# Kernel optimization log

Measured on AMD Instinct MI355X. Metric: run time of the kernel, lower is better.

Reference implementation:

```python
import jax, jax.numpy as jnp
import numpy as np

EPS = 1e-7          # keras K.epsilon()
MIN_TEMP = 0.1
ALPHA = 0.99999
START_TEMP = 10.0
BATCH, D, BINS, K_OUT = 4096, 20000, 10, 64


def setup_inputs() -> dict:
    key = jax.random.key(0)
    k1, k2, k3 = jax.random.split(key, 3)
    X = jax.random.normal(k1, (BATCH, D), dtype=jnp.float32)
    u = jax.random.normal(k2, (D, BINS), dtype=jnp.float32)
    # keras 'uniform' initializer: U(-0.05, 0.05)
    tinyW = jax.random.uniform(k3, (BINS, K_OUT), dtype=jnp.float32, minval=-0.05, maxval=0.05)
    temp = jnp.float32(START_TEMP)
    return {"X": X, "u": u, "tinyW": tinyW, "temp": temp}


def greedy_assign(p):
    """Greedy bipartite argmax-and-mask assignment (the host loop in the original).
    p: (k, d) scores. Returns (k, d) 0/1 assignment with one 1 per row, unique cols."""
    k, d = p.shape

    def step(pm, _):
        ind = jnp.argmax(pm)            # global argmax over flattened (k, d)
        x = ind // d
        y = ind % d
        pm = pm.at[x, :].set(-1.0).at[:, y].set(-1.0)
        return pm, (x, y)

    _, (xs, ys) = jax.lax.scan(step, p, None, length=k)
    return jnp.zeros((k, d), p.dtype).at[xs, ys].set(1.0)


def reference(X, u, tinyW, temp):
    # al = softmax(u @ tinyW) over output_dim axis, then transpose -> (k, d)
    al = jax.nn.softmax(u @ tinyW, axis=-1).T                  # (k, d)
    logits = jnp.log(10.0 * jnp.clip(al, EPS, 0.9999999))      # (k, d)
    # Gumbel noise: -log(-log(U)), U ~ Uniform(eps, 1)
    nkey = jax.random.key(42)
    uniform = jax.random.uniform(nkey, logits.shape, logits.dtype, EPS, 1.0)
    gumbel = -jnp.log(-jnp.log(uniform))
    # annealed temperature update (K.update in original)
    new_temp = jnp.maximum(jnp.float32(MIN_TEMP), temp * jnp.float32(ALPHA))
    samples = jax.nn.softmax((logits + gumbel) / new_temp, axis=-1)  # (k, d)
    # inference-path discrete selection via greedy argmax-and-mask loop
    discrete = greedy_assign(samples)                           # (k, d)
    # training path: Y = X @ samples^T  (main memory-bound skinny GEMM)
    Y = X @ samples.T                                           # (batch, k)
    return Y, discrete, new_temp
```

## Files before the change

kernel.cpp:

```cpp
#include <hip/hip_runtime.h>
#include <stdint.h>
#include <math.h>

typedef unsigned long long ull;
typedef __attribute__((ext_vector_type(8))) short short8;
typedef __attribute__((ext_vector_type(4))) float f32x4;

#define DD 20000
#define NK 64
#define NB 4096
#define YN (NB * NK)
#define TOTN (YN + NK * DD + 1)
#define KS 16

#define E_OFF   0u
#define RSP_OFF 10240000u
#define CV_OFF  10400256u
#define CC_OFF  10416640u
#define EB_OFF  10433024u
#define IRS_OFF 12993024u
#define P_OFF   12993280u

__device__ __forceinline__ uint32_t tf_bits(uint32_t j) {
  const uint32_t k0 = 0u, k1 = 42u;
  const uint32_t k2 = 0x1BD11BDAu ^ k0 ^ k1;
  uint32_t x0 = k0;
  uint32_t x1 = j + k1;
#define TFR(r) { x0 += x1; x1 = (x1 << r) | (x1 >> (32 - r)); x1 ^= x0; }
  TFR(13) TFR(15) TFR(26) TFR(6)
  x0 += k1; x1 += k2 + 1u;
  TFR(17) TFR(29) TFR(16) TFR(24)
  x0 += k2; x1 += k0 + 2u;
  TFR(13) TFR(15) TFR(26) TFR(6)
  x0 += k0; x1 += k1 + 3u;
  TFR(17) TFR(29) TFR(16) TFR(24)
  x0 += k1; x1 += k2 + 4u;
  TFR(13) TFR(15) TFR(26) TFR(6)
  x0 += k2; x1 += k0 + 5u;
#undef TFR
  return x0 ^ x1;
}

__global__ __launch_bounds__(256) void k_z(
    const float* __restrict__ uu, const float* __restrict__ tw,
    const float* __restrict__ temp, double* __restrict__ E,
    ushort* __restrict__ EB, double* __restrict__ RSP,
    float* __restrict__ disc) {
  __shared__ double tile[NK][65];
  __shared__ double psumw[4][NK];
  const int tid = threadIdx.x;
  const int lane = tid & 63;
  const int wv = tid >> 6;
  const int d0 = blockIdx.x * 64;
  const float nt = fmaxf(0.1f, temp[0] * 0.99999f);
  float w[10];
#pragma unroll
  for (int i = 0; i < 10; ++i) w[i] = tw[i * NK + lane];
  double psum = 0.0;
  for (int it = 0; it < 16; ++it) {
    const int dl = wv * 16 + it;
    const int d = d0 + dl;
    double e = 0.0;
    if (d < DD) {
      float m = 0.f;
#pragma unroll
      for (int i = 0; i < 10; ++i) m = fmaf(uu[d * 10 + i], w[i], m);
      float mx = m;
#pragma unroll
      for (int off = 32; off; off >>= 1) mx = fmaxf(mx, __shfl_xor(mx, off, 64));
      double ee = exp((double)(m - mx));
      double ssum = ee;
#pragma unroll
      for (int off = 32; off; off >>= 1) ssum += __shfl_xor(ssum, off, 64);
      float al = (float)(ee / ssum);
      float c = fminf(fmaxf(al, 1e-7f), 0.9999999f);
      float lg = (float)log((double)(10.0f * c));
      const uint32_t bits = tf_bits((uint32_t)(lane * DD + d));
      float uf = __uint_as_float((bits >> 9) | 0x3f800000u) - 1.0f;
      float uv = fmaxf(1e-7f, uf * (1.0f - 1e-7f) + 1e-7f);
      float g = (float)(-log(-log((double)uv)));
      float z = (lg + g) / nt;
      e = exp((double)z);
    }
    tile[lane][dl] = e;
    psum += e;
  }
  psumw[wv][lane] = psum;
  __syncthreads();
  for (int r0 = 0; r0 < NK; r0 += 4) {
    const int r = r0 + wv;
    const int d = d0 + lane;
    if (d < DD) {
      const double ev = tile[r][lane];
      E[(size_t)r * DD + d] = ev;
      const float ef = (float)ev;
      uint32_t ub = __float_as_uint(ef);
      EB[(size_t)r * DD + d] = (ushort)((ub + 0x7FFFu + ((ub >> 16) & 1u)) >> 16);
    }
  }
  if (wv == 0) {
    double s = psumw[0][lane] + psumw[1][lane] + psumw[2][lane] + psumw[3][lane];
    RSP[(size_t)blockIdx.x * NK + lane] = s;
  }
  const int cg = tid & 15;
  const int r0 = tid >> 4;
  if (d0 + cg * 4 < DD) {
    for (int r = r0; r < NK; r += 16)
      *(float4*)(disc + (size_t)r * DD + d0 + cg * 4) = make_float4(0.f, 0.f, 0.f, 0.f);
  }
}

__global__ __launch_bounds__(256) void k_rows(
    const double* __restrict__ E, const double* __restrict__ RSP,
    float* __restrict__ cv, int* __restrict__ cc, float* __restrict__ invRS) {
  const int k = blockIdx.x;
  const int tid = threadIdx.x;
  __shared__ double redd[256];
  __shared__ ull keys[2048];
  __shared__ ull wbest[4];
  const double* er = E + (size_t)k * DD;
  double psum = 0.0;
  for (int b = tid; b < 313; b += 256) psum += RSP[(size_t)b * NK + k];
  redd[tid] = psum;
  __syncthreads();
  for (int s = 128; s; s >>= 1) {
    if (tid < s) redd[tid] += redd[tid + s];
    __syncthreads();
  }
  const double sumall = redd[0];
  if (tid == 0) invRS[k] = (float)(1.0 / sumall);
  float tv[8]; int tc[8];
#pragma unroll
  for (int s = 0; s < 8; ++s) { tv[s] = -1.f; tc[s] = 0; }
  for (int d = tid; d < DD; d += 256) {
    float svv = (float)(er[d] / sumall);
    if (svv > tv[7]) {
      float cvr = svv; int ccr = d;
#pragma unroll
      for (int s = 0; s < 8; ++s) {
        bool sw = cvr > tv[s];
        float nv = sw ? cvr : tv[s]; int nc = sw ? ccr : tc[s];
        cvr = sw ? tv[s] : cvr; ccr = sw ? tc[s] : ccr;
        tv[s] = nv; tc[s] = nc;
      }
    }
  }
#pragma unroll
  for (int s = 0; s < 8; ++s)
    keys[(tid << 3) + s] = (((ull)__float_as_uint(tv[s])) << 32)
                         | ((ull)(uint32_t)(32767 - tc[s]) << 11)
                         | ((ull)tid << 3) | (ull)s;
  __syncthreads();
  for (int t = 0; t < NK; ++t) {
    ull best = 0;
#pragma unroll
    for (int s = 0; s < 8; ++s) { ull kk = keys[(tid << 3) + s]; if (kk > best) best = kk; }
#pragma unroll
    for (int off = 32; off; off >>= 1) { ull o = __shfl_xor(best, off, 64); if (o > best) best = o; }
    if ((tid & 63) == 0) wbest[tid >> 6] = best;
    __syncthreads();
    ull win = wbest[0];
#pragma unroll
    for (int wI = 1; wI < 4; ++wI) if (wbest[wI] > win) win = wbest[wI];
    const uint32_t lo = (uint32_t)win;
    const int slot = lo & 7;
    const int owner = (lo >> 3) & 255;
    const int col = 32767 - (int)(lo >> 11);
    if (tid == 0) {
      cv[(k << 6) + t] = __uint_as_float((uint32_t)(win >> 32));
      cc[(k << 6) + t] = col;
    }
    if (tid == owner) keys[(owner << 3) + slot] = 0;
    __syncthreads();
  }
}

__global__ __launch_bounds__(64) void k_greedy(
    const float* __restrict__ cv, const int* __restrict__ cc,
    const float* __restrict__ temp, float* __restrict__ out) {
  __shared__ float vf[NK * NK];
  __shared__ int cf[NK * NK];
  __shared__ unsigned char used[DD];
  const int lane = threadIdx.x;
  for (int i = lane; i < DD; i += 64) used[i] = 0;
  for (int i = lane; i < 1024; i += 64) {
    ((float4*)vf)[i] = ((const float4*)cv)[i];
    ((int4*)cf)[i] = ((const int4*)cc)[i];
  }
  __syncthreads();
  int ptr = 0;
  bool done = false;
  for (int t = 0; t < NK; ++t) {
    ull key = 0;
    if (!done) {
      while (ptr < NK && used[cf[(lane << 6) + ptr]]) ++ptr;
      if (ptr < NK) {
        key = (((ull)__float_as_uint(vf[(lane << 6) + ptr])) << 21)
            | ((ull)(uint32_t)(63 - lane) << 15)
            | (ull)(uint32_t)(32767 - cf[(lane << 6) + ptr]);
      }
    }
#pragma unroll
    for (int off = 32; off; off >>= 1) { ull o = __shfl_xor(key, off, 64); if (o > key) key = o; }
    const int col = 32767 - (int)(key & 0x7FFF);
    const int row = 63 - (int)((key >> 15) & 63);
    if (lane == row) done = true;
    if (lane == 0) { used[col] = 1; out[YN + (size_t)row * DD + col] = 1.0f; }
    __syncthreads();
  }
  if (lane == 0) out[TOTN - 1] = fmaxf(0.1f, temp[0] * 0.99999f);
}

__global__ __launch_bounds__(256) void k_gemm(
    const float* __restrict__ X, const ushort* __restrict__ EB,
    float* __restrict__ P) {
  const int tid = threadIdx.x;
  const int lane = tid & 63;
  const int wv = tid >> 6;
  const int ksp = blockIdx.x;
  const int m16 = lane & 15;
  const int kq = lane >> 4;
  const int mRow = blockIdx.y * 64 + wv * 16 + m16;
  const float* xp = X + (size_t)mRow * DD;
  const ushort* bp = EB + (size_t)m16 * DD;
  f32x4 acc[4] = {{0,0,0,0},{0,0,0,0},{0,0,0,0},{0,0,0,0}};
#pragma unroll 2
  for (int s = ksp; s < 625; s += KS) {
    const int k0 = s * 32 + kq * 8;
    const float4 xa = *(const float4*)(xp + k0);
    const float4 xb = *(const float4*)(xp + k0 + 4);
    union { uint4 q[4]; short8 v[4]; } B;
#pragma unroll
    for (int nt = 0; nt < 4; ++nt)
      B.q[nt] = *(const uint4*)(bp + (size_t)nt * 16 * DD + k0);
    union { uint32_t u[4]; short8 v; } A;
    uint32_t ua0 = __float_as_uint(xa.x), ua1 = __float_as_uint(xa.y);
    uint32_t ua2 = __float_as_uint(xa.z), ua3 = __float_as_uint(xa.w);
    uint32_t ub0 = __float_as_uint(xb.x), ub1 = __float_as_uint(xb.y);
    uint32_t ub2 = __float_as_uint(xb.z), ub3 = __float_as_uint(xb.w);
    ua0 = (ua0 + 0x7FFFu + ((ua0 >> 16) & 1u)) >> 16;
    ua1 = (ua1 + 0x7FFFu + ((ua1 >> 16) & 1u)) >> 16;
    ua2 = (ua2 + 0x7FFFu + ((ua2 >> 16) & 1u)) >> 16;
    ua3 = (ua3 + 0x7FFFu + ((ua3 >> 16) & 1u)) >> 16;
    ub0 = (ub0 + 0x7FFFu + ((ub0 >> 16) & 1u)) >> 16;
    ub1 = (ub1 + 0x7FFFu + ((ub1 >> 16) & 1u)) >> 16;
    ub2 = (ub2 + 0x7FFFu + ((ub2 >> 16) & 1u)) >> 16;
    ub3 = (ub3 + 0x7FFFu + ((ub3 >> 16) & 1u)) >> 16;
    A.u[0] = ua0 | (ua1 << 16); A.u[1] = ua2 | (ua3 << 16);
    A.u[2] = ub0 | (ub1 << 16); A.u[3] = ub2 | (ub3 << 16);
#pragma unroll
    for (int nt = 0; nt < 4; ++nt)
      acc[nt] = __builtin_amdgcn_mfma_f32_16x16x32_bf16(A.v, B.v[nt], acc[nt], 0, 0, 0);
  }
  float* pp = P + (size_t)ksp * YN;
  const int rBase = blockIdx.y * 64 + wv * 16 + kq * 4;
#pragma unroll
  for (int nt = 0; nt < 4; ++nt)
#pragma unroll
    for (int r = 0; r < 4; ++r)
      pp[(size_t)(rBase + r) * 64 + nt * 16 + m16] = acc[nt][r];
}

__global__ __launch_bounds__(256) void k_gred(const float* __restrict__ P,
                                              const float* __restrict__ invRS,
                                              float* __restrict__ Y) {
  const int i = blockIdx.x * 256 + threadIdx.x;
  float4 a = ((const float4*)P)[i];
#pragma unroll
  for (int j = 1; j < KS; ++j) {
    const float4 b = ((const float4*)(P + (size_t)j * YN))[i];
    a.x += b.x; a.y += b.y; a.z += b.z; a.w += b.w;
  }
  const float4 irs = *(const float4*)(invRS + ((i * 4) & 63));
  a.x *= irs.x; a.y *= irs.y; a.z *= irs.z; a.w *= irs.w;
  ((float4*)Y)[i] = a;
}

extern "C" void kernel_launch(void* const* d_in, const int* in_sizes, int n_in,
                              void* d_out, int out_size, void* d_ws, size_t ws_size,
                              hipStream_t stream) {
  (void)in_sizes; (void)n_in; (void)out_size; (void)ws_size;
  const float* X = (const float*)d_in[0];
  const float* uu = (const float*)d_in[1];
  const float* tw = (const float*)d_in[2];
  const float* temp = (const float*)d_in[3];
  float* out = (float*)d_out;
  char* W = (char*)d_ws;
  double* E   = (double*)(W + E_OFF);
  double* RSP = (double*)(W + RSP_OFF);
  float*  CV  = (float*)(W + CV_OFF);
  int*    CC  = (int*)(W + CC_OFF);
  ushort* EB  = (ushort*)(W + EB_OFF);
  float*  IRS = (float*)(W + IRS_OFF);
  float*  P   = (float*)(W + P_OFF);

  hipLaunchKernelGGL(k_z, dim3(313), dim3(256), 0, stream, uu, tw, temp, E, EB, RSP, out + YN);
  hipLaunchKernelGGL(k_gemm, dim3(KS, 64), dim3(256), 0, stream, X, EB, P);
  hipLaunchKernelGGL(k_rows, dim3(64), dim3(256), 0, stream, E, RSP, CV, CC, IRS);
  hipLaunchKernelGGL(k_greedy, dim3(1), dim3(64), 0, stream, CV, CC, temp, out);
  hipLaunchKernelGGL(k_gred, dim3(256), dim3(256), 0, stream, P, IRS, out);
}
```

Baseline: 650.4 us.

## Merge row top-k into GEMM launch, pipeline GEMM loads, merge greedy with reduction

The row top-k kernel is folded into the GEMM launch as 64 extra blocks, so the serial per-row selection overlaps with the memory-bound GEMM. The greedy assignment and the split-K reduction now share one launch, cutting the launch count from five to three. The GEMM inner loop gains explicit triple-buffered register prefetching of X and the bf16 E tiles, and the greedy loop is rewritten around a ballot/shuffle argmax that keeps one cached candidate per row. The costs are higher register pressure in the GEMM and a single serial greedy block that may still sit on the critical path.

```diff
diff --git a/kernel.cpp b/kernel.cpp
--- a/kernel.cpp
+++ b/kernel.cpp
@@ -110,150 +110,134 @@
   }
 }
 
-__global__ __launch_bounds__(256) void k_rows(
+__global__ __launch_bounds__(256) void k_gr(
+    const float* __restrict__ X, const ushort* __restrict__ EB,
+    float* __restrict__ P,
     const double* __restrict__ E, const double* __restrict__ RSP,
     float* __restrict__ cv, int* __restrict__ cc, float* __restrict__ invRS) {
-  const int k = blockIdx.x;
   const int tid = threadIdx.x;
-  __shared__ double redd[256];
-  __shared__ ull keys[2048];
-  __shared__ ull wbest[4];
-  const double* er = E + (size_t)k * DD;
-  double psum = 0.0;
-  for (int b = tid; b < 313; b += 256) psum += RSP[(size_t)b * NK + k];
-  redd[tid] = psum;
-  __syncthreads();
-  for (int s = 128; s; s >>= 1) {
-    if (tid < s) redd[tid] += redd[tid + s];
+  if (blockIdx.x < 64) {
+    const int k = blockIdx.x;
+    __shared__ double redd[256];
+    __shared__ ull keys[2048];
+    __shared__ ull wbest[4];
+    const double* er = E + (size_t)k * DD;
+    double psum = 0.0;
+    for (int b = tid; b < 313; b += 256) psum += RSP[(size_t)b * NK + k];
+    redd[tid] = psum;
     __syncthreads();
-  }
-  const double sumall = redd[0];
-  if (tid == 0) invRS[k] = (float)(1.0 / sumall);
-  float tv[8]; int tc[8];
-#pragma unroll
-  for (int s = 0; s < 8; ++s) { tv[s] = -1.f; tc[s] = 0; }
-  for (int d = tid; d < DD; d += 256) {
-    float svv = (float)(er[d] / sumall);
-    if (svv > tv[7]) {
-      float cvr = svv; int ccr = d;
-#pragma unroll
-      for (int s = 0; s < 8; ++s) {
-        bool sw = cvr > tv[s];
-        float nv = sw ? cvr : tv[s]; int nc = sw ? ccr : tc[s];
-        cvr = sw ? tv[s] : cvr; ccr = sw ? tc[s] : ccr;
-        tv[s] = nv; tc[s] = nc;
+    for (int s = 128; s; s >>= 1) {
+      if (tid < s) redd[tid] += redd[tid + s];
+      __syncthreads();
+    }
+    const double sumall = redd[0];
+    if (tid == 0) invRS[k] = (float)(1.0 / sumall);
+    float tv[8]; int tc[8];
+#pragma unroll
+    for (int s = 0; s < 8; ++s) { tv[s] = -1.f; tc[s] = 0; }
+    for (int d = tid; d < DD; d += 256) {
+      float svv = (float)(er[d] / sumall);
+      if (svv > tv[7]) {
+        float cvr = svv; int ccr = d;
+#pragma unroll
+        for (int s = 0; s < 8; ++s) {
+          bool sw = cvr > tv[s];
+          float nv = sw ? cvr : tv[s]; int nc = sw ? ccr : tc[s];
+          cvr = sw ? tv[s] : cvr; ccr = sw ? tc[s] : ccr;
+          tv[s] = nv; tc[s] = nc;
+        }
       }
     }
-  }
-#pragma unroll
-  for (int s = 0; s < 8; ++s)
-    keys[(tid << 3) + s] = (((ull)__float_as_uint(tv[s])) << 32)
-                         | ((ull)(uint32_t)(32767 - tc[s]) << 11)
-                         | ((ull)tid << 3) | (ull)s;
-  __syncthreads();
-  for (int t = 0; t < NK; ++t) {
-    ull best = 0;
-#pragma unroll
-    for (int s = 0; s < 8; ++s) { ull kk = keys[(tid << 3) + s]; if (kk > best) best = kk; }
-#pragma unroll
-    for (int off = 32; off; off >>= 1) { ull o = __shfl_xor(best, off, 64); if (o > best) best = o; }
-    if ((tid & 63) == 0) wbest[tid >> 6] = best;
+#pragma unroll
+    for (int s = 0; s < 8; ++s)
+      keys[(tid << 3) + s] = (((ull)__float_as_uint(tv[s])) << 32)
+                           | ((ull)(uint32_t)(32767 - tc[s]) << 11)
+                           | ((ull)tid << 3) | (ull)s;
     __syncthreads();
-    ull win = wbest[0];
-#pragma unroll
-    for (int wI = 1; wI < 4; ++wI) if (wbest[wI] > win) win = wbest[wI];
-    const uint32_t lo = (uint32_t)win;
-    const int slot = lo & 7;
-    const int owner = (lo >> 3) & 255;
-    const int col = 32767 - (int)(lo >> 11);
-    if (tid == 0) {
-      cv[(k << 6) + t] = __uint_as_float((uint32_t)(win >> 32));
-      cc[(k << 6) + t] = col;
-    }
-    if (tid == owner) keys[(owner << 3) + slot] = 0;
-    __syncthreads();
-  }
-}
-
-__global__ __launch_bounds__(64) void k_greedy(
-    const float* __restrict__ cv, const int* __restrict__ cc,
-    const float* __restrict__ temp, float* __restrict__ out) {
-  __shared__ float vf[NK * NK];
-  __shared__ int cf[NK * NK];
-  __shared__ unsigned char used[DD];
-  const int lane = threadIdx.x;
-  for (int i = lane; i < DD; i += 64) used[i] = 0;
-  for (int i = lane; i < 1024; i += 64) {
-    ((float4*)vf)[i] = ((const float4*)cv)[i];
-    ((int4*)cf)[i] = ((const int4*)cc)[i];
-  }
-  __syncthreads();
-  int ptr = 0;
-  bool done = false;
-  for (int t = 0; t < NK; ++t) {
-    ull key = 0;
-    if (!done) {
-      while (ptr < NK && used[cf[(lane << 6) + ptr]]) ++ptr;
-      if (ptr < NK) {
-        key = (((ull)__float_as_uint(vf[(lane << 6) + ptr])) << 21)
-            | ((ull)(uint32_t)(63 - lane) << 15)
-            | (ull)(uint32_t)(32767 - cf[(lane << 6) + ptr]);
+    for (int t = 0; t < NK; ++t) {
+      ull best = 0;
+#pragma unroll
+      for (int s = 0; s < 8; ++s) { ull kk = keys[(tid << 3) + s]; if (kk > best) best = kk; }
+#pragma unroll
+      for (int off = 32; off; off >>= 1) { ull o = __shfl_xor(best, off, 64); if (o > best) best = o; }
+      if ((tid & 63) == 0) wbest[tid >> 6] = best;
+      __syncthreads();
+      ull win = wbest[0];
+#pragma unroll
+      for (int wI = 1; wI < 4; ++wI) if (wbest[wI] > win) win = wbest[wI];
+      const uint32_t lo = (uint32_t)win;
+      const int slot = lo & 7;
+      const int owner = (lo >> 3) & 255;
+      const int col = 32767 - (int)(lo >> 11);
+      if (tid == 0) {
+        cv[(k << 6) + t] = __uint_as_float((uint32_t)(win >> 32));
+        cc[(k << 6) + t] = col;
       }
-    }
-#pragma unroll
-    for (int off = 32; off; off >>= 1) { ull o = __shfl_xor(key, off, 64); if (o > key) key = o; }
-    const int col = 32767 - (int)(key & 0x7FFF);
-    const int row = 63 - (int)((key >> 15) & 63);
-    if (lane == row) done = true;
-    if (lane == 0) { used[col] = 1; out[YN + (size_t)row * DD + col] = 1.0f; }
-    __syncthreads();
-  }
-  if (lane == 0) out[TOTN - 1] = fmaxf(0.1f, temp[0] * 0.99999f);
-}
-
-__global__ __launch_bounds__(256) void k_gemm(
-    const float* __restrict__ X, const ushort* __restrict__ EB,
-    float* __restrict__ P) {
-  const int tid = threadIdx.x;
+      if (tid == owner) keys[(owner << 3) + slot] = 0;
+      __syncthreads();
+    }
+    return;
+  }
+  const int bx2 = blockIdx.x - 64;
+  const int ksp = bx2 >> 6;
+  const int by = bx2 & 63;
   const int lane = tid & 63;
   const int wv = tid >> 6;
-  const int ksp = blockIdx.x;
   const int m16 = lane & 15;
   const int kq = lane >> 4;
-  const int mRow = blockIdx.y * 64 + wv * 16 + m16;
-  const float* xp = X + (size_t)mRow * DD;
-  const ushort* bp = EB + (size_t)m16 * DD;
+  const int mRow = by * 64 + wv * 16 + m16;
+  const float* xq = X + (size_t)mRow * DD + ksp * 32 + kq * 8;
+  const ushort* bq = EB + (size_t)m16 * DD + ksp * 32 + kq * 8;
   f32x4 acc[4] = {{0,0,0,0},{0,0,0,0},{0,0,0,0},{0,0,0,0}};
-#pragma unroll 2
-  for (int s = ksp; s < 625; s += KS) {
-    const int k0 = s * 32 + kq * 8;
-    const float4 xa = *(const float4*)(xp + k0);
-    const float4 xb = *(const float4*)(xp + k0 + 4);
-    union { uint4 q[4]; short8 v[4]; } B;
-#pragma unroll
-    for (int nt = 0; nt < 4; ++nt)
-      B.q[nt] = *(const uint4*)(bp + (size_t)nt * 16 * DD + k0);
-    union { uint32_t u[4]; short8 v; } A;
-    uint32_t ua0 = __float_as_uint(xa.x), ua1 = __float_as_uint(xa.y);
-    uint32_t ua2 = __float_as_uint(xa.z), ua3 = __float_as_uint(xa.w);
-    uint32_t ub0 = __float_as_uint(xb.x), ub1 = __float_as_uint(xb.y);
-    uint32_t ub2 = __float_as_uint(xb.z), ub3 = __float_as_uint(xb.w);
-    ua0 = (ua0 + 0x7FFFu + ((ua0 >> 16) & 1u)) >> 16;
-    ua1 = (ua1 + 0x7FFFu + ((ua1 >> 16) & 1u)) >> 16;
-    ua2 = (ua2 + 0x7FFFu + ((ua2 >> 16) & 1u)) >> 16;
-    ua3 = (ua3 + 0x7FFFu + ((ua3 >> 16) & 1u)) >> 16;
-    ub0 = (ub0 + 0x7FFFu + ((ub0 >> 16) & 1u)) >> 16;
-    ub1 = (ub1 + 0x7FFFu + ((ub1 >> 16) & 1u)) >> 16;
-    ub2 = (ub2 + 0x7FFFu + ((ub2 >> 16) & 1u)) >> 16;
-    ub3 = (ub3 + 0x7FFFu + ((ub3 >> 16) & 1u)) >> 16;
-    A.u[0] = ua0 | (ua1 << 16); A.u[1] = ua2 | (ua3 << 16);
-    A.u[2] = ub0 | (ub1 << 16); A.u[3] = ub2 | (ub3 << 16);
-#pragma unroll
-    for (int nt = 0; nt < 4; ++nt)
-      acc[nt] = __builtin_amdgcn_mfma_f32_16x16x32_bf16(A.v, B.v[nt], acc[nt], 0, 0, 0);
-  }
+  const int jN = (625 - ksp + KS - 1) / KS;
+
+#define LOADBUF(xa, xb, bn, j) { \
+    const int o_ = (j) * (KS * 32); \
+    xa = *(const float4*)(xq + o_); \
+    xb = *(const float4*)(xq + o_ + 4); \
+    bn##0 = *(const uint4*)(bq + o_); \
+    bn##1 = *(const uint4*)(bq + 16 * DD + o_); \
+    bn##2 = *(const uint4*)(bq + 32 * DD + o_); \
+    bn##3 = *(const uint4*)(bq + 48 * DD + o_); }
+
+#define COMPUTEBUF(xa, xb, bn) { \
+    uint32_t t0=__float_as_uint(xa.x), t1=__float_as_uint(xa.y), t2=__float_as_uint(xa.z), t3=__float_as_uint(xa.w); \
+    uint32_t t4=__float_as_uint(xb.x), t5=__float_as_uint(xb.y), t6=__float_as_uint(xb.z), t7=__float_as_uint(xb.w); \
+    t0=(t0+0x7FFFu+((t0>>16)&1u))>>16; t1=(t1+0x7FFFu+((t1>>16)&1u))>>16; \
+    t2=(t2+0x7FFFu+((t2>>16)&1u))>>16; t3=(t3+0x7FFFu+((t3>>16)&1u))>>16; \
+    t4=(t4+0x7FFFu+((t4>>16)&1u))>>16; t5=(t5+0x7FFFu+((t5>>16)&1u))>>16; \
+    t6=(t6+0x7FFFu+((t6>>16)&1u))>>16; t7=(t7+0x7FFFu+((t7>>16)&1u))>>16; \
+    union { uint32_t u[4]; short8 v; } A_; \
+    A_.u[0]=t0|(t1<<16); A_.u[1]=t2|(t3<<16); A_.u[2]=t4|(t5<<16); A_.u[3]=t6|(t7<<16); \
+    union { uint4 q; short8 v; } Q0_, Q1_, Q2_, Q3_; \
+    Q0_.q = bn##0; Q1_.q = bn##1; Q2_.q = bn##2; Q3_.q = bn##3; \
+    acc[0] = __builtin_amdgcn_mfma_f32_16x16x32_bf16(A_.v, Q0_.v, acc[0], 0, 0, 0); \
+    acc[1] = __builtin_amdgcn_mfma_f32_16x16x32_bf16(A_.v, Q1_.v, acc[1], 0, 0, 0); \
+    acc[2] = __builtin_amdgcn_mfma_f32_16x16x32_bf16(A_.v, Q2_.v, acc[2], 0, 0, 0); \
+    acc[3] = __builtin_amdgcn_mfma_f32_16x16x32_bf16(A_.v, Q3_.v, acc[3], 0, 0, 0); }
+
+  float4 xaA, xbA, xaB, xbB, xaC, xbC;
+  uint4 bA0, bA1, bA2, bA3, bB0, bB1, bB2, bB3, bC0, bC1, bC2, bC3;
+  LOADBUF(xaA, xbA, bA, 0);
+  LOADBUF(xaB, xbB, bB, 1);
+  LOADBUF(xaC, xbC, bC, 2);
+  int j = 0;
+  for (; j + 3 < jN; j += 3) {
+    COMPUTEBUF(xaA, xbA, bA);
+    LOADBUF(xaA, xbA, bA, j + 3);
+    COMPUTEBUF(xaB, xbB, bB);
+    if (j + 4 < jN) { LOADBUF(xaB, xbB, bB, j + 4); }
+    COMPUTEBUF(xaC, xbC, bC);
+    if (j + 5 < jN) { LOADBUF(xaC, xbC, bC, j + 5); }
+  }
+  COMPUTEBUF(xaA, xbA, bA);
+  if (j + 1 < jN) { COMPUTEBUF(xaB, xbB, bB); }
+  if (j + 2 < jN) { COMPUTEBUF(xaC, xbC, bC); }
+#undef LOADBUF
+#undef COMPUTEBUF
+
   float* pp = P + (size_t)ksp * YN;
-  const int rBase = blockIdx.y * 64 + wv * 16 + kq * 4;
+  const int rBase = by * 64 + wv * 16 + kq * 4;
 #pragma unroll
   for (int nt = 0; nt < 4; ++nt)
 #pragma unroll
@@ -261,10 +245,56 @@
       pp[(size_t)(rBase + r) * 64 + nt * 16 + m16] = acc[nt][r];
 }
 
-__global__ __launch_bounds__(256) void k_gred(const float* __restrict__ P,
-                                              const float* __restrict__ invRS,
-                                              float* __restrict__ Y) {
-  const int i = blockIdx.x * 256 + threadIdx.x;
+__global__ __launch_bounds__(256) void k_tail(
+    const float* __restrict__ cv, const int* __restrict__ cc,
+    const float* __restrict__ temp, const float* __restrict__ P,
+    const float* __restrict__ invRS, float* __restrict__ out) {
+  const int tid = threadIdx.x;
+  if (blockIdx.x == 0) {
+    __shared__ float vf[NK * NK];
+    __shared__ int cf[NK * NK];
+    __shared__ alignas(16) unsigned char used[DD];
+    for (int i = tid; i < 1250; i += 256) ((int4*)used)[i] = make_int4(0, 0, 0, 0);
+    for (int i = tid; i < 1024; i += 256) {
+      ((float4*)vf)[i] = ((const float4*)cv)[i];
+      ((int4*)cf)[i] = ((const int4*)cc)[i];
+    }
+    __syncthreads();
+    if (tid >= 64) return;
+    const int lane = tid;
+    int ptr = 0;
+    float hv = vf[lane << 6];
+    int hc = cf[lane << 6];
+    bool done = false;
+    for (int t = 0; t < NK; ++t) {
+      const float v = done ? -1.f : hv;
+      float m = v;
+#pragma unroll
+      for (int off = 32; off; off >>= 1) m = fmaxf(m, __shfl_xor(m, off, 64));
+      const ull mask = __ballot(v == m);
+      const int row = __ffsll(mask) - 1;
+      const int col = __shfl(hc, row, 64);
+      if (lane == row) done = true;
+      if (lane == 0) {
+        used[col] = 1;
+        out[YN + (size_t)row * DD + col] = 1.0f;
+      }
+      asm volatile("s_waitcnt lgkmcnt(0)" ::: "memory");
+      if (!done && hc == col) {
+        ++ptr;
+        while (ptr < NK) {
+          hc = cf[(lane << 6) + ptr];
+          if (!used[hc]) break;
+          ++ptr;
+        }
+        if (ptr < NK) hv = vf[(lane << 6) + ptr];
+        else { hv = -2.f; hc = 0; }
+      }
+    }
+    if (lane == 0) out[TOTN - 1] = fmaxf(0.1f, temp[0] * 0.99999f);
+    return;
+  }
+  const int i = (blockIdx.x - 1) * 256 + tid;
   float4 a = ((const float4*)P)[i];
 #pragma unroll
   for (int j = 1; j < KS; ++j) {
@@ -273,7 +303,7 @@
   }
   const float4 irs = *(const float4*)(invRS + ((i * 4) & 63));
   a.x *= irs.x; a.y *= irs.y; a.z *= irs.z; a.w *= irs.w;
-  ((float4*)Y)[i] = a;
+  ((float4*)out)[i] = a;
 }
 
 extern "C" void kernel_launch(void* const* d_in, const int* in_sizes, int n_in,
@@ -295,8 +325,6 @@
   float*  P   = (float*)(W + P_OFF);
 
   hipLaunchKernelGGL(k_z, dim3(313), dim3(256), 0, stream, uu, tw, temp, E, EB, RSP, out + YN);
-  hipLaunchKernelGGL(k_gemm, dim3(KS, 64), dim3(256), 0, stream, X, EB, P);
-  hipLaunchKernelGGL(k_rows, dim3(64), dim3(256), 0, stream, E, RSP, CV, CC, IRS);
-  hipLaunchKernelGGL(k_greedy, dim3(1), dim3(64), 0, stream, CV, CC, temp, out);
-  hipLaunchKernelGGL(k_gred, dim3(256), dim3(256), 0, stream, P, IRS, out);
-}
+  hipLaunchKernelGGL(k_gr, dim3(64 + KS * 64), dim3(256), 0, stream, X, EB, P, E, RSP, CV, CC, IRS);
+  hipLaunchKernelGGL(k_tail, dim3(257), dim3(256), 0, stream, CV, CC, temp, P, IRS, out);
+}
```

New measurement: 559.9 us. 1.16x faster.
